# Kernel optimization log

Measured on AMD Instinct MI355X. Metric: run time of the kernel, lower is better.

## Reference

```python
import jax, jax.numpy as jnp
import numpy as np

EMB = 1024

def setup_inputs() -> dict:
    key = jax.random.key(0)
    ks = jax.random.split(key, 10)
    B, S, E = 8, 2048, EMB
    x = jax.random.normal(ks[0], (B, S, E), dtype=jnp.float32)
    context = jax.random.normal(ks[1], (B, S, E), dtype=jnp.float32)
    pad_mask = jax.random.randint(ks[2], (B, S, S), 0, 2) == 1
    s = 1.0 / np.sqrt(E)
    Wq = jax.random.normal(ks[3], (E, E), dtype=jnp.float32) * s
    bq = jnp.zeros((E,), dtype=jnp.float32)
    Wk = jax.random.normal(ks[4], (E, E), dtype=jnp.float32) * s
    bk = jnp.zeros((E,), dtype=jnp.float32)
    Wv = jax.random.normal(ks[5], (E, E), dtype=jnp.float32) * s
    bv = jnp.zeros((E,), dtype=jnp.float32)
    return {"x": x, "context": context, "pad_mask": pad_mask,
            "Wq": Wq, "bq": bq, "Wk": Wk, "bk": bk, "Wv": Wv, "bv": bv}

def reference(x, context, pad_mask, Wq, bq, Wk, bk, Wv, bv):
    scale = x.shape[-1] ** (-0.5)
    Q = jnp.einsum('bse,fe->bsf', x, Wq) + bq
    K = jnp.einsum('bse,fe->bsf', context, Wk) + bk
    V = jnp.einsum('bse,fe->bsf', context, Wv) + bv
    att = jnp.einsum('bid,bjd->bij', Q, K) * scale
    att = jnp.where(pad_mask, jnp.float32(-1e9), att)
    att = jax.nn.softmax(att, axis=-1)
    out = jnp.einsum('bij,bjk->bik', att, V)
    return (out, att)
```

## Files before the change

### kernel.cpp

```cpp
#include <hip/hip_runtime.h>
#include <hip/hip_bf16.h>
#include <type_traits>

typedef __attribute__((ext_vector_type(8))) __bf16 bf16x8;
typedef __attribute__((ext_vector_type(4))) float f32x4;
typedef unsigned short u16;

__device__ __forceinline__ u16 f2b(float x) {
  union { __hip_bfloat16 b; u16 u; } cv;
  cv.b = __float2bfloat16(x);
  return cv.u;
}

__device__ __forceinline__ void ld16(const u16* g, u16* l) {
  __builtin_amdgcn_global_load_lds(
      (const __attribute__((address_space(1))) unsigned int*)g,
      (__attribute__((address_space(3))) unsigned int*)l, 16, 0, 0);
}

constexpr int BM = 128, BN = 128, BK = 64;

enum { EPI_NONE = 0, EPI_BIAS = 1, EPI_BIAS_T = 2, EPI_MASK = 3 };

template <typename TC, int EPI>
__global__ __launch_bounds__(256) void gemm_bt(
    const u16* __restrict__ A, const u16* __restrict__ Bt, TC* __restrict__ C,
    const float* __restrict__ bias, const int* __restrict__ mask, float scale,
    int N, int K, long long sA, long long sB, long long sC, long long sM) {
  __shared__ u16 As[BM * BK];
  __shared__ u16 Bs[BN * BK];

  const int bz = blockIdx.z;
  A += (size_t)bz * sA;
  Bt += (size_t)bz * sB;
  C += (size_t)bz * sC;
  const long long maskBase = (long long)bz * sM;

  const int m0 = blockIdx.y * BM, n0 = blockIdx.x * BN;
  const int t = threadIdx.x, wave = t >> 6, lane = t & 63;
  const int wm = (wave >> 1) * 64, wn = (wave & 1) * 64;
  const int fr = lane & 15, quad = lane >> 4;

  const int lr = lane >> 3, lc = lane & 7;
  const int cg = (lc ^ lr) * 8;
  const u16* ga = A + (size_t)(m0 + wave * 32 + lr) * K + cg;
  const u16* gb = Bt + (size_t)(n0 + wave * 32 + lr) * K + cg;

  f32x4 acc[4][4] = {};

  for (int k0 = 0; k0 < K; k0 += BK) {
#pragma unroll
    for (int p = 0; p < 4; ++p) {
      ld16(ga + (size_t)(8 * p) * K, &As[(wave * 32 + 8 * p) * BK]);
      ld16(gb + (size_t)(8 * p) * K, &Bs[(wave * 32 + 8 * p) * BK]);
    }
    ga += BK;
    gb += BK;
    __builtin_amdgcn_s_waitcnt(0x0f70);
    __syncthreads();

#pragma unroll
    for (int ks = 0; ks < 2; ++ks) {
      bf16x8 af[4], bfr[4];
#pragma unroll
      for (int i = 0; i < 4; ++i)
        af[i] = *(const bf16x8*)
            &As[(wm + i * 16 + fr) * BK + (((ks * 4 + quad) ^ (fr & 7)) * 8)];
#pragma unroll
      for (int j = 0; j < 4; ++j)
        bfr[j] = *(const bf16x8*)
            &Bs[(wn + j * 16 + fr) * BK + (((ks * 4 + quad) ^ (fr & 7)) * 8)];
#pragma unroll
      for (int i = 0; i < 4; ++i)
#pragma unroll
        for (int j = 0; j < 4; ++j)
          acc[i][j] = __builtin_amdgcn_mfma_f32_16x16x32_bf16(
              af[i], bfr[j], acc[i][j], 0, 0, 0);
    }
    __syncthreads();
  }

#pragma unroll
  for (int i = 0; i < 4; ++i)
#pragma unroll
    for (int j = 0; j < 4; ++j) {
      const int mb = m0 + wm + i * 16 + quad * 4;
      const int n = n0 + wn + j * 16 + fr;
      if constexpr (EPI == EPI_BIAS_T) {
        const float bb = bias[n];
        const int b = mb >> 11, ml = mb & 2047;
        ushort4 o;
        o.x = f2b(acc[i][j][0] + bb);
        o.y = f2b(acc[i][j][1] + bb);
        o.z = f2b(acc[i][j][2] + bb);
        o.w = f2b(acc[i][j][3] + bb);
        *(ushort4*)&((u16*)C)[(size_t)b * 2097152 + (size_t)n * 2048 + ml] = o;
      } else {
#pragma unroll
        for (int r = 0; r < 4; ++r) {
          const int m = mb + r;
          float v = acc[i][j][r];
          if constexpr (EPI == EPI_BIAS) v += bias[n];
          if constexpr (EPI == EPI_MASK)
            v = mask[maskBase + (size_t)m * N + n] ? -1e9f : v * scale;
          if constexpr (std::is_same_v<TC, u16>)
            C[(size_t)m * N + n] = f2b(v);
          else
            C[(size_t)m * N + n] = v;
        }
      }
    }
}

__global__ __launch_bounds__(256) void cast_all(
    const float* __restrict__ x, const float* __restrict__ ctx,
    const float* __restrict__ wq, const float* __restrict__ wk,
    const float* __restrict__ wv, u16* __restrict__ xb, u16* __restrict__ cb,
    u16* __restrict__ wqb, u16* __restrict__ wkb, u16* __restrict__ wvb) {
  int b = blockIdx.x;
  const float* s;
  u16* d;
  size_t off;
  if (b < 16384) { s = x; d = xb; off = b; }
  else if (b < 32768) { s = ctx; d = cb; off = b - 32768 + 16384; }
  else if (b < 33792) { s = wq; d = wqb; off = b - 32768; }
  else if (b < 34816) { s = wk; d = wkb; off = b - 33792; }
  else { s = wv; d = wvb; off = b - 34816; }
  const size_t i = (off * 256 + threadIdx.x) * 4;
  float4 v = *(const float4*)&s[i];
  ushort4 h;
  h.x = f2b(v.x); h.y = f2b(v.y); h.z = f2b(v.z); h.w = f2b(v.w);
  *(ushort4*)&d[i] = h;
}

__device__ __forceinline__ float blockReduceMax(float v, float* red) {
#pragma unroll
  for (int o = 32; o > 0; o >>= 1) v = fmaxf(v, __shfl_down(v, o));
  int t = threadIdx.x;
  if ((t & 63) == 0) red[t >> 6] = v;
  __syncthreads();
  float r = fmaxf(fmaxf(red[0], red[1]), fmaxf(red[2], red[3]));
  __syncthreads();
  return r;
}

__device__ __forceinline__ float blockReduceSum(float v, float* red) {
#pragma unroll
  for (int o = 32; o > 0; o >>= 1) v += __shfl_down(v, o);
  int t = threadIdx.x;
  if ((t & 63) == 0) red[t >> 6] = v;
  __syncthreads();
  float r = red[0] + red[1] + red[2] + red[3];
  __syncthreads();
  return r;
}

__global__ __launch_bounds__(256) void softmax_rows(float* __restrict__ att,
                                                    u16* __restrict__ attb) {
  __shared__ float red[4];
  float* p = att + (size_t)blockIdx.x * 2048;
  u16* pb = attb + (size_t)blockIdx.x * 2048;
  const int t = threadIdx.x;
  float4 v0 = ((const float4*)p)[t];
  float4 v1 = ((const float4*)p)[t + 256];
  float mx = fmaxf(fmaxf(fmaxf(v0.x, v0.y), fmaxf(v0.z, v0.w)),
                   fmaxf(fmaxf(v1.x, v1.y), fmaxf(v1.z, v1.w)));
  mx = blockReduceMax(mx, red);
  float4 e0, e1;
  e0.x = __expf(v0.x - mx); e0.y = __expf(v0.y - mx);
  e0.z = __expf(v0.z - mx); e0.w = __expf(v0.w - mx);
  e1.x = __expf(v1.x - mx); e1.y = __expf(v1.y - mx);
  e1.z = __expf(v1.z - mx); e1.w = __expf(v1.w - mx);
  float s = (e0.x + e0.y + e0.z + e0.w) + (e1.x + e1.y + e1.z + e1.w);
  s = blockReduceSum(s, red);
  float inv = 1.0f / s;
  e0.x *= inv; e0.y *= inv; e0.z *= inv; e0.w *= inv;
  e1.x *= inv; e1.y *= inv; e1.z *= inv; e1.w *= inv;
  ((float4*)p)[t] = e0;
  ((float4*)p)[t + 256] = e1;
  ushort4 h0, h1;
  h0.x = f2b(e0.x); h0.y = f2b(e0.y); h0.z = f2b(e0.z); h0.w = f2b(e0.w);
  h1.x = f2b(e1.x); h1.y = f2b(e1.y); h1.z = f2b(e1.z); h1.w = f2b(e1.w);
  *(ushort4*)&pb[(size_t)t * 4] = h0;
  *(ushort4*)&pb[(size_t)(t + 256) * 4] = h1;
}

extern "C" void kernel_launch(void* const* d_in, const int* in_sizes, int n_in,
                              void* d_out, int out_size, void* d_ws,
                              size_t ws_size, hipStream_t stream) {
  const float* x   = (const float*)d_in[0];
  const float* ctx = (const float*)d_in[1];
  const int*   msk = (const int*)d_in[2];
  const float* Wq  = (const float*)d_in[3];
  const float* bq  = (const float*)d_in[4];
  const float* Wk  = (const float*)d_in[5];
  const float* bk  = (const float*)d_in[6];
  const float* Wv  = (const float*)d_in[7];
  const float* bv  = (const float*)d_in[8];

  float* out = (float*)d_out;
  float* att = out + 16777216;

  u16* xb = (u16*)d_ws;
  u16* cb = xb + 16777216;
  u16* Q  = cb + 16777216;
  u16* Kb = Q + 16777216;
  u16* Vt = xb;
  u16* attb = Q;
  u16* wqb = (u16*)att;
  u16* wkb = wqb + 1048576;
  u16* wvb = wkb + 1048576;

  dim3 blk(256);
  const long long SQ = 2048LL * 1024, SS = 2048LL * 2048, SV = 1024LL * 2048;

  cast_all<<<dim3(35840), blk, 0, stream>>>(x, ctx, Wq, Wk, Wv, xb, cb, wqb,
                                            wkb, wvb);

  gemm_bt<u16, EPI_BIAS><<<dim3(8, 128, 1), blk, 0, stream>>>(
      xb, wqb, Q, bq, nullptr, 0.f, 1024, 1024, 0, 0, 0, 0);
  gemm_bt<u16, EPI_BIAS><<<dim3(8, 128, 1), blk, 0, stream>>>(
      cb, wkb, Kb, bk, nullptr, 0.f, 1024, 1024, 0, 0, 0, 0);
  gemm_bt<u16, EPI_BIAS_T><<<dim3(8, 128, 1), blk, 0, stream>>>(
      cb, wvb, Vt, bv, nullptr, 0.f, 1024, 1024, 0, 0, 0, 0);

  gemm_bt<float, EPI_MASK><<<dim3(16, 16, 8), blk, 0, stream>>>(
      Q, Kb, att, nullptr, msk, 0.03125f, 2048, 1024, SQ, SQ, SS, SS);

  softmax_rows<<<dim3(16384), blk, 0, stream>>>(att, attb);

  gemm_bt<float, EPI_NONE><<<dim3(8, 16, 8), blk, 0, stream>>>(
      attb, Vt, out, nullptr, nullptr, 0.f, 1024, 2048, SS, SV, SQ, 0);
}
```

Baseline: 782.0 us.

## Use 256x256 tiles with double-buffered LDS and phased MFMA scheduling

The GEMM kernel grows from 128x128 tiles with 4 waves to 256x256 tiles with 8 waves, and keeps two LDS buffers so the global-to-LDS loads for tile k+2 are issued while tile k is being computed. The inner loop is split into four phases with explicit barriers and setprio around the MFMA bursts, and fragments are reused across phases to cut LDS reads. The goal is to hide load latency and raise arithmetic intensity. The cost is 128KB of LDS per block and a much smaller grid: the projection GEMMs get 256 blocks, which can hurt occupancy and leave CUs idle.

```diff
diff --git a/kernel.cpp b/kernel.cpp
--- a/kernel.cpp
+++ b/kernel.cpp
@@ -18,17 +18,46 @@
       (__attribute__((address_space(3))) unsigned int*)l, 16, 0, 0);
 }
 
-constexpr int BM = 128, BN = 128, BK = 64;
+constexpr int BM = 256, BN = 256, BK = 64;
 
 enum { EPI_NONE = 0, EPI_BIAS = 1, EPI_BIAS_T = 2, EPI_MASK = 3 };
 
+#define PHASE(QR, QC, LA, LB, BUF)                                            \
+  {                                                                           \
+    if (LA) {                                                                 \
+      _Pragma("unroll") for (int i = 0; i < 4; ++i)                           \
+          _Pragma("unroll") for (int ks = 0; ks < 2; ++ks)                    \
+              aF[i][ks] = *(const bf16x8*)&As[BUF][                           \
+                  (wr * 128 + QR * 64 + i * 16 + fr) * BK +                   \
+                  (((ks * 4 + quad) ^ (fr & 7)) * 8)];                        \
+    }                                                                         \
+    if (LB) {                                                                 \
+      _Pragma("unroll") for (int j = 0; j < 2; ++j)                           \
+          _Pragma("unroll") for (int ks = 0; ks < 2; ++ks)                    \
+              bF[j][ks] = *(const bf16x8*)&Bs[BUF][                           \
+                  (wc * 64 + QC * 32 + j * 16 + fr) * BK +                    \
+                  (((ks * 4 + quad) ^ (fr & 7)) * 8)];                        \
+    }                                                                         \
+    __builtin_amdgcn_s_barrier();                                             \
+    __builtin_amdgcn_s_setprio(1);                                            \
+    _Pragma("unroll") for (int i = 0; i < 4; ++i)                             \
+        _Pragma("unroll") for (int j = 0; j < 2; ++j)                         \
+            _Pragma("unroll") for (int ks = 0; ks < 2; ++ks)                  \
+                acc[QR * 4 + i][QC * 2 + j] =                                 \
+                    __builtin_amdgcn_mfma_f32_16x16x32_bf16(                  \
+                        aF[i][ks], bF[j][ks], acc[QR * 4 + i][QC * 2 + j],    \
+                        0, 0, 0);                                             \
+    __builtin_amdgcn_s_setprio(0);                                            \
+    __builtin_amdgcn_s_barrier();                                             \
+  }
+
 template <typename TC, int EPI>
-__global__ __launch_bounds__(256) void gemm_bt(
+__global__ __launch_bounds__(512, 2) void gemm_bt(
     const u16* __restrict__ A, const u16* __restrict__ Bt, TC* __restrict__ C,
     const float* __restrict__ bias, const int* __restrict__ mask, float scale,
     int N, int K, long long sA, long long sB, long long sC, long long sM) {
-  __shared__ u16 As[BM * BK];
-  __shared__ u16 Bs[BN * BK];
+  __shared__ u16 As[2][BM * BK];
+  __shared__ u16 Bs[2][BN * BK];
 
   const int bz = blockIdx.z;
   A += (size_t)bz * sA;
@@ -38,54 +67,56 @@
 
   const int m0 = blockIdx.y * BM, n0 = blockIdx.x * BN;
   const int t = threadIdx.x, wave = t >> 6, lane = t & 63;
-  const int wm = (wave >> 1) * 64, wn = (wave & 1) * 64;
+  const int wr = wave >> 2, wc = wave & 3;
   const int fr = lane & 15, quad = lane >> 4;
-
   const int lr = lane >> 3, lc = lane & 7;
-  const int cg = (lc ^ lr) * 8;
-  const u16* ga = A + (size_t)(m0 + wave * 32 + lr) * K + cg;
-  const u16* gb = Bt + (size_t)(n0 + wave * 32 + lr) * K + cg;
-
-  f32x4 acc[4][4] = {};
-
-  for (int k0 = 0; k0 < K; k0 += BK) {
-#pragma unroll
-    for (int p = 0; p < 4; ++p) {
-      ld16(ga + (size_t)(8 * p) * K, &As[(wave * 32 + 8 * p) * BK]);
-      ld16(gb + (size_t)(8 * p) * K, &Bs[(wave * 32 + 8 * p) * BK]);
+
+  const u16* ga = A + (size_t)(m0 + wave * 8 + lr) * K + (lc ^ lr) * 8;
+  const u16* gb = Bt + (size_t)(n0 + wave * 8 + lr) * K + (lc ^ lr) * 8;
+
+  f32x4 acc[8][4] = {};
+  bf16x8 aF[4][2], bF[2][2];
+
+  const int nt = K / BK;
+
+  auto STAGE = [&](int kt, int bsel) {
+    const size_t ko = (size_t)kt * BK;
+#pragma unroll
+    for (int i = 0; i < 4; ++i) {
+      ld16(ga + (size_t)(i * 64) * K + ko,
+           &As[bsel][(i * 64 + wave * 8) * BK]);
+      ld16(gb + (size_t)(i * 64) * K + ko,
+           &Bs[bsel][(i * 64 + wave * 8) * BK]);
     }
-    ga += BK;
-    gb += BK;
-    __builtin_amdgcn_s_waitcnt(0x0f70);
-    __syncthreads();
-
-#pragma unroll
-    for (int ks = 0; ks < 2; ++ks) {
-      bf16x8 af[4], bfr[4];
-#pragma unroll
-      for (int i = 0; i < 4; ++i)
-        af[i] = *(const bf16x8*)
-            &As[(wm + i * 16 + fr) * BK + (((ks * 4 + quad) ^ (fr & 7)) * 8)];
-#pragma unroll
-      for (int j = 0; j < 4; ++j)
-        bfr[j] = *(const bf16x8*)
-            &Bs[(wn + j * 16 + fr) * BK + (((ks * 4 + quad) ^ (fr & 7)) * 8)];
-#pragma unroll
-      for (int i = 0; i < 4; ++i)
-#pragma unroll
-        for (int j = 0; j < 4; ++j)
-          acc[i][j] = __builtin_amdgcn_mfma_f32_16x16x32_bf16(
-              af[i], bfr[j], acc[i][j], 0, 0, 0);
-    }
-    __syncthreads();
+  };
+
+  STAGE(0, 0);
+  STAGE(1, 1);
+
+  for (int kt = 0; kt < nt; ++kt) {
+    const int b = kt & 1;
+    if (kt + 1 < nt)
+      __builtin_amdgcn_s_waitcnt(0x0f78);
+    else
+      __builtin_amdgcn_s_waitcnt(0x0f70);
+    __builtin_amdgcn_s_barrier();
+    __builtin_amdgcn_sched_barrier(0);
+
+    PHASE(0, 0, 1, 1, b)
+    PHASE(0, 1, 0, 1, b)
+    PHASE(1, 1, 1, 0, b)
+    PHASE(1, 0, 0, 1, b)
+
+    __builtin_amdgcn_sched_barrier(0);
+    if (kt + 2 < nt) STAGE(kt + 2, b);
   }
 
 #pragma unroll
-  for (int i = 0; i < 4; ++i)
+  for (int i = 0; i < 8; ++i)
 #pragma unroll
     for (int j = 0; j < 4; ++j) {
-      const int mb = m0 + wm + i * 16 + quad * 4;
-      const int n = n0 + wn + j * 16 + fr;
+      const int mb = m0 + wr * 128 + i * 16 + quad * 4;
+      const int n = n0 + wc * 64 + j * 16 + fr;
       if constexpr (EPI == EPI_BIAS_T) {
         const float bb = bias[n];
         const int b = mb >> 11, ml = mb & 2047;
@@ -211,24 +242,24 @@
   u16* wkb = wqb + 1048576;
   u16* wvb = wkb + 1048576;
 
-  dim3 blk(256);
+  dim3 blk(256), blkg(512);
   const long long SQ = 2048LL * 1024, SS = 2048LL * 2048, SV = 1024LL * 2048;
 
   cast_all<<<dim3(35840), blk, 0, stream>>>(x, ctx, Wq, Wk, Wv, xb, cb, wqb,
                                             wkb, wvb);
 
-  gemm_bt<u16, EPI_BIAS><<<dim3(8, 128, 1), blk, 0, stream>>>(
+  gemm_bt<u16, EPI_BIAS><<<dim3(4, 64, 1), blkg, 0, stream>>>(
       xb, wqb, Q, bq, nullptr, 0.f, 1024, 1024, 0, 0, 0, 0);
-  gemm_bt<u16, EPI_BIAS><<<dim3(8, 128, 1), blk, 0, stream>>>(
+  gemm_bt<u16, EPI_BIAS><<<dim3(4, 64, 1), blkg, 0, stream>>>(
       cb, wkb, Kb, bk, nullptr, 0.f, 1024, 1024, 0, 0, 0, 0);
-  gemm_bt<u16, EPI_BIAS_T><<<dim3(8, 128, 1), blk, 0, stream>>>(
+  gemm_bt<u16, EPI_BIAS_T><<<dim3(4, 64, 1), blkg, 0, stream>>>(
       cb, wvb, Vt, bv, nullptr, 0.f, 1024, 1024, 0, 0, 0, 0);
 
-  gemm_bt<float, EPI_MASK><<<dim3(16, 16, 8), blk, 0, stream>>>(
+  gemm_bt<float, EPI_MASK><<<dim3(8, 8, 8), blkg, 0, stream>>>(
       Q, Kb, att, nullptr, msk, 0.03125f, 2048, 1024, SQ, SQ, SS, SS);
 
   softmax_rows<<<dim3(16384), blk, 0, stream>>>(att, attb);
 
-  gemm_bt<float, EPI_NONE><<<dim3(8, 16, 8), blk, 0, stream>>>(
+  gemm_bt<float, EPI_NONE><<<dim3(4, 8, 8), blkg, 0, stream>>>(
       attb, Vt, out, nullptr, nullptr, 0.f, 1024, 2048, SS, SV, SQ, 0);
 }
```

Result: faster. 749.4 us (-4.2%).
